# Kernel tuning notes

Measured on AMD Instinct MI355X. Metric: run time of the kernel, lower is better.

## Reference

```python
import math
from functools import partial

import jax
import jax.numpy as jnp
import numpy as np

DS = 128            # domain_size (cells per side); original used 600
PD = 1.0            # particle diameter d == grid spacing
KN = 500000.0       # normal stiffness
MASS = 1.0
DT = 1e-4
FS = 5              # filter (stencil) size -> 5x5x5 shifts
_ALPHA = -math.log(0.7) / math.pi
_GAMMA = _ALPHA / math.sqrt(_ALPHA ** 2 + 1.0)
ETA = 2.0 * _GAMMA * math.sqrt(KN * MASS)   # damping_coefficient_Eta
EPS = 1e-4          # torch.clamp(dist, 0.0001)
SHAPE = (1, 1, DS, DS, DS)


def setup_inputs() -> dict:
    rng = np.random.default_rng(0)
    occ = np.zeros((DS, DS, DS), np.float32)
    occ[1:-1, 1:-1, 1:-1] = (rng.random((DS - 2,) * 3) < 0.2).astype(np.float32)
    iz, iy, ix = np.meshgrid(np.arange(DS), np.arange(DS), np.arange(DS), indexing="ij")
    jit = lambda: (rng.random((DS,) * 3).astype(np.float32) - 0.5) * 0.4
    # occupied cells store their own coordinate (+jitter) so round(x/d) == cell index
    x = (occ * (ix.astype(np.float32) + jit())).astype(np.float32)
    y = (occ * (iy.astype(np.float32) + jit())).astype(np.float32)
    z = (occ * (iz.astype(np.float32) + jit())).astype(np.float32)
    vel = lambda: (occ * rng.normal(0.0, 0.5, (DS,) * 3)).astype(np.float32)
    asg = lambda a: jnp.asarray(a.reshape(SHAPE))
    return {
        "x_grid": asg(x), "y_grid": asg(y), "z_grid": asg(z),
        "vx_grid": asg(vel()), "vy_grid": asg(vel()), "vz_grid": asg(vel()),
        "mask": asg(occ),
    }


def _contrib(xg, yg, zg, vxg, vyg, vzg, shift):
    """Force contribution from one (i,j,k) stencil shift (torch.roll based)."""
    roll = lambda g: jnp.roll(g, shift, axis=(2, 3, 4))
    dx, dy, dz = xg - roll(xg), yg - roll(yg), zg - roll(zg)
    sq = dx * dx + dy * dy + dz * dz
    dist = jnp.sqrt(sq + 1e-20)  # tiny eps keeps sqrt grad finite at sq==0; value unchanged in fp32
    cd = jnp.maximum(dist, EPS)  # torch.clamp(dist, 0.0001)
    vn = ((vxg - roll(vxg)) * dx + (vyg - roll(vyg)) * dy + (vzg - roll(vzg)) * dz) / cd
    ov = dist < 2.0 * PD
    fx = jnp.where(ov, KN * (dist - 2.0 * PD) * dx / cd + ETA * vn * dx / cd, 0.0)
    fy = jnp.where(ov, KN * (dist - 2.0 * PD) * dy / cd + ETA * vn * dy / cd, 0.0)
    fz = jnp.where(ov, KN * (dist - 2.0 * PD) * dz / cd + ETA * vn * dz / cd, 0.0)
    return fx, fy, fz


def _forward(xg, yg, zg, vxg, vyg, vzg, mask):
    f32 = jnp.float32
    fx = jnp.zeros(SHAPE, f32)
    fy = jnp.zeros(SHAPE, f32)
    fz = jnp.zeros(SHAPE, f32)
    for i in range(FS):
        for j in range(FS):
            for k in range(FS):
                c = jax.checkpoint(partial(_contrib, shift=(k - 2, j - 2, i - 2)))
                dfx, dfy, dfz = c(xg, yg, zg, vxg, vyg, vzg)
                fx, fy, fz = fx + dfx, fy + dfy, fz + dfz
    # boundary overlap forces
    bl = ((xg != 0.0) & (xg < PD)).astype(f32)
    br = (xg > DS - 2.0 * PD).astype(f32)
    bb = ((yg != 0.0) & (yg < PD)).astype(f32)
    bt = (yg > DS - 2.0 * PD).astype(f32)
    bf = ((zg != 0.0) & (zg < PD)).astype(f32)
    bk = (zg > DS - 2.0 * PD).astype(f32)
    fxb = KN * bl * mask * (PD - xg) - KN * br * mask * (xg - DS + 2.0 * PD) - ETA * vxg * bl * mask - ETA * vxg * br * mask
    fyb = KN * bb * mask * (PD - yg) - KN * bt * mask * (yg - DS + 2.0 * PD) - ETA * vyg * bb * mask - ETA * vyg * bt * mask
    fzb = KN * bf * mask * (PD - zg) - KN * bk * mask * (zg - DS + 2.0 * PD) - ETA * vzg * bf * mask - ETA * vzg * bk * mask
    vxn = vxg + DT / MASS * mask * (-0.0 * MASS - fx + fxb)
    vyn = vyg + DT / MASS * mask * (-9.8 * MASS - fy + fyb)
    vzn = vzg + DT / MASS * mask * (-0.0 * MASS - fz + fzb)
    cell = lambda g: jnp.round(g / PD).astype(jnp.int32)
    cx0, cy0, cz0 = cell(xg), cell(yg), cell(zg)
    xn, yn, zn = xg + DT * vxn, yg + DT * vyn, zg + DT * vzn
    cx1, cy1, cz1 = cell(xn), cell(yn), cell(zn)
    # cell-list relocation: flatten to linear indices; invalid (empty) cells -> dump slot D3
    D3 = DS ** 3
    def lin(cz, cy, cx):
        v = (cx != 0) & (cy != 0) & (cz != 0)   # torch filters cell_* != 0
        return jnp.where(v, (cz * DS + cy) * DS + cx, D3).reshape(-1)
    lo = lin(cz0, cy0, cx0)
    ln = lin(cz1, cy1, cx1)
    pad = lambda g: jnp.concatenate([g.reshape(-1), jnp.zeros((1,), g.dtype)])
    unpad = lambda f: f[:D3].reshape(SHAPE)
    def move(g):
        gf = pad(g)
        return unpad(gf.at[lo].set(0.0).at[ln].set(gf[lo]))
    mask_n = unpad(pad(mask).at[lo].set(0.0).at[ln].set(1.0))
    return (move(xn), move(yn), move(zn), move(vxn), move(vyn), move(vzn), mask_n)


def reference(x_grid, y_grid, z_grid, vx_grid, vy_grid, vz_grid, mask):
    return _forward(x_grid, y_grid, z_grid, vx_grid, vy_grid, vz_grid, mask)
```

## Files before the change

kernel.cpp:

```cpp
#include <hip/hip_runtime.h>

#define DSZ   128
#define DMSK  127
#define D3    (DSZ * DSZ * DSZ)

#define KN_F   500000.0f
#define ETA_F  159.535258f
#define DT_F   1e-4f

#define TBX   32
#define TBY   4
#define TBZ   4
#define HALO  2
#define HX    36
#define RS    37
#define PS    296
#define SLOTS 2368
#define NT    512

struct OffTabs { int inc[84]; int exc[44]; };
constexpr OffTabs make_tabs() {
    OffTabs t{}; int a = 0, e = 0;
    for (int dz = -2; dz <= 2; ++dz)
        for (int dy = -2; dy <= 2; ++dy)
            for (int dx = -2; dx <= 2; ++dx) {
                const int off = dz * PS + dy * RS + dx;
                if (dz*dz + dy*dy + dx*dx <= 6) t.inc[a++] = off;
                else                            t.exc[e++] = off;
            }
    while (a < 84) t.inc[a++] = 0;
    return t;
}
__constant__ OffTabs g_tabs = make_tabs();

typedef float f4a4 __attribute__((ext_vector_type(4), aligned(4)));

__device__ __forceinline__ unsigned bf16_rne(float f) {
    unsigned u = __float_as_uint(f);
    u += 0x7fffu + ((u >> 16) & 1u);
    return u >> 16;
}
__device__ __forceinline__ unsigned packvv(float vy, float vz) {
    return bf16_rne(vy) | (bf16_rne(vz) << 16);
}
__device__ __forceinline__ float unpk_lo(unsigned w) { return __uint_as_float(w << 16); }
__device__ __forceinline__ float unpk_hi(unsigned w) { return __uint_as_float(w & 0xffff0000u); }

__device__ __forceinline__ void pair_full(
    const float4* __restrict__ lsp, const unsigned* __restrict__ lsv, int n,
    float px, float py, float pz, float vx, float vy, float vz,
    float& fx, float& fy, float& fz)
{
    const float4 q = lsp[n];
    const float ddx = px - q.x, ddy = py - q.y, ddz = pz - q.z;
    const float sq  = ddx*ddx + ddy*ddy + ddz*ddz;
    const float dist = sqrtf(sq + 1e-20f);
    const float rcd  = __builtin_amdgcn_rcpf(fmaxf(dist, 1e-4f));
    const unsigned w = lsv[n];
    const float vn = ((vx - q.w)*ddx + (vy - unpk_lo(w))*ddy + (vz - unpk_hi(w))*ddz) * rcd;
    float coef = (KN_F * (dist - 2.0f) + ETA_F * vn) * rcd;
    coef = (dist < 2.0f) ? coef : 0.0f;
    fx = fmaf(coef, ddx, fx);
    fy = fmaf(coef, ddy, fy);
    fz = fmaf(coef, ddz, fz);
}

__device__ __forceinline__ void store_cell(float* __restrict__ out, int idx,
    float xn, float yn, float zn, float vxn, float vyn, float vzn, float mk)
{
    out[idx]          = xn;
    out[idx + 1 * D3] = yn;
    out[idx + 2 * D3] = zn;
    out[idx + 3 * D3] = vxn;
    out[idx + 4 * D3] = vyn;
    out[idx + 5 * D3] = vzn;
    out[idx + 6 * D3] = mk;
}

__device__ __forceinline__ void store7_sub(float* __restrict__ out, int idx,
    float x, float y, float z, float vx, float vy, float vz, float mk, int sub)
{
    const float a = (sub == 0) ? x : (sub == 1) ? y : (sub == 2) ? z : vx;
    out[idx + sub * D3] = a;
    if (sub < 3) {
        const float b = (sub == 0) ? vy : (sub == 1) ? vz : mk;
        out[idx + (sub + 4) * D3] = b;
    }
}

__device__ __forceinline__ void write_reloc(float* __restrict__ out, int c, int lo, int ln,
    float xn, float yn, float zn, float vxn, float vyn, float vzn, float mask_in)
{
    if (ln == lo) {
        store_cell(out, c, xn, yn, zn, vxn, vyn, vzn, (ln < D3) ? 1.0f : mask_in);
    } else {
        float sx = xn, sy = yn, sz = zn, svx = vxn, svy = vyn, svz = vzn;
        if (lo < D3) {
            store_cell(out, lo, 0.f, 0.f, 0.f, 0.f, 0.f, 0.f, 0.0f);
        } else {
            store_cell(out, c, xn, yn, zn, vxn, vyn, vzn, mask_in);
            sx = sy = sz = svx = svy = svz = 0.f;
        }
        if (ln < D3) store_cell(out, ln, sx, sy, sz, svx, svy, svz, 1.0f);
    }
}

__device__ __forceinline__ void write_reloc_sub(float* __restrict__ out, int c, int lo, int ln,
    float xn, float yn, float zn, float vxn, float vyn, float vzn, int sub)
{
    if (ln == lo) {
        store7_sub(out, c, xn, yn, zn, vxn, vyn, vzn, 1.0f, sub);
    } else {
        float sx = xn, sy = yn, sz = zn, svx = vxn, svy = vyn, svz = vzn;
        if (lo < D3) {
            store7_sub(out, lo, 0.f, 0.f, 0.f, 0.f, 0.f, 0.f, 0.f, sub);
        } else {
            store7_sub(out, c, xn, yn, zn, vxn, vyn, vzn, 1.0f, sub);
            sx = sy = sz = svx = svy = svz = 0.f;
        }
        if (ln < D3) store7_sub(out, ln, sx, sy, sz, svx, svy, svz, 1.0f, sub);
    }
}

__device__ __forceinline__ void integrate_store(float* __restrict__ out, int c,
    float px, float py, float pz, float vxn, float vyn, float vzn, float mask_in)
{
    const float xn = px + DT_F * vxn;
    const float yn = py + DT_F * vyn;
    const float zn = pz + DT_F * vzn;
    const int cx0 = (int)rintf(px), cy0 = (int)rintf(py), cz0 = (int)rintf(pz);
    const int cx1 = (int)rintf(xn), cy1 = (int)rintf(yn), cz1 = (int)rintf(zn);
    const int lo = (cx0 != 0 && cy0 != 0 && cz0 != 0) ? ((cz0 * DSZ + cy0) * DSZ + cx0) : D3;
    const int ln = (cx1 != 0 && cy1 != 0 && cz1 != 0) ? ((cz1 * DSZ + cy1) * DSZ + cx1) : D3;
    write_reloc(out, c, lo, ln, xn, yn, zn, vxn, vyn, vzn, mask_in);
}

__global__ __launch_bounds__(NT) void dem_tile(
    const float* __restrict__ X, const float* __restrict__ Y, const float* __restrict__ Z,
    const float* __restrict__ VX, const float* __restrict__ VY, const float* __restrict__ VZ,
    float* __restrict__ out)
{
    __shared__ float4 lsp[SLOTS];
    __shared__ unsigned lsv[SLOTS];
    __shared__ unsigned short plist[NT];
    __shared__ int loff[128];
    __shared__ unsigned int pcnt;

    const int tid = threadIdx.x;

    const unsigned raw = blockIdx.x;
    const unsigned xcd = raw & 7, loc = raw >> 3;
    const int bx = (int)((loc & 3) * TBX);
    const int by = (int)(((loc >> 2) & 31) * TBY);
    const int bz = (int)((xcd * 4 + (loc >> 7)) * TBZ);

    if (tid == 0) pcnt = 0;
    if (tid < 84) loff[tid] = g_tabs.inc[tid];
    else if (tid < 128) loff[tid] = g_tabs.exc[tid - 84];

    if (bx == 32 || bx == 64) {
        for (int u = tid; u < 2880; u += NT) {
            if (u < 2304) {
                const int f = u & 3;
                const int t = u >> 2;
                const int qw = t % 9;
                const int r = t / 9;
                const int hz = r >> 3, hy = r & 7;
                const int gz = (bz + hz - HALO) & DMSK;
                const int gy = (by + hy - HALO) & DMSK;
                const float* F = (f == 0) ? X : (f == 1) ? Y : (f == 2) ? Z : VX;
                const f4a4 a = *(const f4a4*)(F + (gz * DSZ + gy) * DSZ + (bx - HALO) + qw * 4);
                float* lb = (float*)lsp + (hz * PS + hy * RS + qw * 4) * 4 + f;
                #pragma unroll
                for (int e = 0; e < 4; ++e) lb[e * 4] = a[e];
            } else {
                const int v = u - 2304;
                const int qw = v % 9;
                const int r = v / 9;
                const int hz = r >> 3, hy = r & 7;
                const int gz = (bz + hz - HALO) & DMSK;
                const int gy = (by + hy - HALO) & DMSK;
                const int gb = (gz * DSZ + gy) * DSZ + (bx - HALO) + qw * 4;
                const f4a4 yv = *(const f4a4*)(VY + gb);
                const f4a4 zv = *(const f4a4*)(VZ + gb);
                unsigned* vb = lsv + hz * PS + hy * RS + qw * 4;
                #pragma unroll
                for (int e = 0; e < 4; ++e) vb[e] = packvv(yv[e], zv[e]);
            }
        }
    } else {
        for (int h = tid; h < 2304; h += NT) {
            const int hx = h % 36;
            const int rr = h / 36;
            const int hy = rr & 7, hz = rr >> 3;
            const int g = (((bz + hz - HALO) & DMSK) * DSZ + ((by + hy - HALO) & DMSK)) * DSZ
                          + ((bx + hx - HALO) & DMSK);
            const int slot = hz * PS + hy * RS + hx;
            lsp[slot] = make_float4(X[g], Y[g], Z[g], VX[g]);
            lsv[slot] = packvv(VY[g], VZ[g]);
        }
    }

    __syncthreads();

    const int tx = tid & 31, ty = (tid >> 5) & 3, tz = tid >> 7;
    const int c = ((bz + tz) * DSZ + (by + ty)) * DSZ + (bx + tx);
    const int lcc = (tz + HALO) * PS + (ty + HALO) * RS + (tx + HALO);
    const float4 qo = lsp[lcc];
    const bool occ = (qo.x != 0.0f);

    {
        const unsigned long long bmask = __ballot(occ);
        const int lane = tid & 63;
        const unsigned int prefix = (unsigned int)__popcll(bmask & ((1ull << lane) - 1ull));
        unsigned int base = 0;
        if (lane == 0) base = atomicAdd(&pcnt, (unsigned int)__popcll(bmask));
        base = __shfl(base, 0, 64);
        if (occ) plist[base + prefix] = (unsigned short)tid;
    }

    if (!occ) {
        const unsigned w = lsv[lcc];
        integrate_store(out, c, qo.x, qo.y, qo.z, qo.w, unpk_lo(w), unpk_hi(w), 0.0f);
    }

    __syncthreads();

    const int n = (int)pcnt;
    const int sub = tid & 3;
    for (int i = tid >> 2; i < n; i += NT / 4) {
        const int p  = plist[i];
        const int px_ = p & 31, py_ = (p >> 5) & 3, pz_ = p >> 7;
        const int lc = (pz_ + HALO) * PS + (py_ + HALO) * RS + (px_ + HALO);
        const int cp = ((bz + pz_) * DSZ + (by + py_)) * DSZ + (bx + px_);

        const float4 qc = lsp[lc];
        const unsigned wc = lsv[lc];
        const float px = qc.x, py = qc.y, pz = qc.z;
        const float vx = qc.w, vy = unpk_lo(wc), vz = unpk_hi(wc);
        float fx = 0.f, fy = 0.f, fz = 0.f;

        #pragma unroll 3
        for (int tt = 0; tt < 21; ++tt)
            pair_full(lsp, lsv, lc + loff[tt * 4 + sub], px, py, pz, vx, vy, vz, fx, fy, fz);

        const float sqo = px*px + py*py + pz*pz;
        if (sqo < 4.0f) {
            for (int t = sub; t < 44; t += 4)
                pair_full(lsp, lsv, lc + loff[84 + t], px, py, pz, vx, vy, vz, fx, fy, fz);
        }

        fx += __shfl_xor(fx, 1); fy += __shfl_xor(fy, 1); fz += __shfl_xor(fz, 1);
        fx += __shfl_xor(fx, 2); fy += __shfl_xor(fy, 2); fz += __shfl_xor(fz, 2);

        const float bl = (px != 0.0f && px < 1.0f)  ? 1.0f : 0.0f;
        const float br = (px > 126.0f)              ? 1.0f : 0.0f;
        const float bb = (py != 0.0f && py < 1.0f)  ? 1.0f : 0.0f;
        const float bt = (py > 126.0f)              ? 1.0f : 0.0f;
        const float bf = (pz != 0.0f && pz < 1.0f)  ? 1.0f : 0.0f;
        const float bk = (pz > 126.0f)              ? 1.0f : 0.0f;
        const float fxb = KN_F * bl * (1.0f - px) - KN_F * br * (px - 126.0f) - ETA_F * vx * (bl + br);
        const float fyb = KN_F * bb * (1.0f - py) - KN_F * bt * (py - 126.0f) - ETA_F * vy * (bb + bt);
        const float fzb = KN_F * bf * (1.0f - pz) - KN_F * bk * (pz - 126.0f) - ETA_F * vz * (bf + bk);

        const float vxn = vx + DT_F * (-fx + fxb);
        const float vyn = vy + DT_F * (-9.8f - fy + fyb);
        const float vzn = vz + DT_F * (-fz + fzb);
        const float xn = px + DT_F * vxn;
        const float yn = py + DT_F * vyn;
        const float zn = pz + DT_F * vzn;

        const int cx0 = (int)rintf(px), cy0 = (int)rintf(py), cz0 = (int)rintf(pz);
        const int cx1 = (int)rintf(xn), cy1 = (int)rintf(yn), cz1 = (int)rintf(zn);
        const int lo = (cx0 != 0 && cy0 != 0 && cz0 != 0) ? ((cz0 * DSZ + cy0) * DSZ + cx0) : D3;
        const int ln = (cx1 != 0 && cy1 != 0 && cz1 != 0) ? ((cz1 * DSZ + cy1) * DSZ + cx1) : D3;

        write_reloc_sub(out, cp, lo, ln, xn, yn, zn, vxn, vyn, vzn, sub);
    }
}

extern "C" void kernel_launch(void* const* d_in, const int* in_sizes, int n_in,
                              void* d_out, int out_size, void* d_ws, size_t ws_size,
                              hipStream_t stream)
{
    const float* X  = (const float*)d_in[0];
    const float* Y  = (const float*)d_in[1];
    const float* Z  = (const float*)d_in[2];
    const float* VX = (const float*)d_in[3];
    const float* VY = (const float*)d_in[4];
    const float* VZ = (const float*)d_in[5];
    float* out = (float*)d_out;

    dem_tile<<<(D3 / (TBX * TBY * TBZ)), NT, 0, stream>>>(X, Y, Z, VX, VY, VZ, out);
}
```

Before: 178.7 us.

## Stage outputs in LDS for coalesced float4 stores and defer relocations

Per-cell results, for both empty cells and occupied particles, are now written into a shared-memory staging buffer that reuses the particle LDS area. They are then written to global memory as coalesced float4 stores per field. Cross-cell relocations are collected in a small shared list and written after the tile store. The halo load is also unified: interior columns use vector loads and the 2-wide x halo uses scalar loads, so there is no longer a special path for some tiles. This replaces scattered per-thread stores, but it caps relocations at 8 per block, silently drops any beyond that, and can change write ordering for relocations that cross tiles.

New measurement: 180.2 us. About the same (+0.8%).

```diff
diff --git a/kernel.cpp b/kernel.cpp
--- a/kernel.cpp
+++ b/kernel.cpp
@@ -12,7 +12,6 @@
 #define TBY   4
 #define TBZ   4
 #define HALO  2
-#define HX    36
 #define RS    37
 #define PS    296
 #define SLOTS 2368
@@ -65,76 +64,6 @@
     fz = fmaf(coef, ddz, fz);
 }
 
-__device__ __forceinline__ void store_cell(float* __restrict__ out, int idx,
-    float xn, float yn, float zn, float vxn, float vyn, float vzn, float mk)
-{
-    out[idx]          = xn;
-    out[idx + 1 * D3] = yn;
-    out[idx + 2 * D3] = zn;
-    out[idx + 3 * D3] = vxn;
-    out[idx + 4 * D3] = vyn;
-    out[idx + 5 * D3] = vzn;
-    out[idx + 6 * D3] = mk;
-}
-
-__device__ __forceinline__ void store7_sub(float* __restrict__ out, int idx,
-    float x, float y, float z, float vx, float vy, float vz, float mk, int sub)
-{
-    const float a = (sub == 0) ? x : (sub == 1) ? y : (sub == 2) ? z : vx;
-    out[idx + sub * D3] = a;
-    if (sub < 3) {
-        const float b = (sub == 0) ? vy : (sub == 1) ? vz : mk;
-        out[idx + (sub + 4) * D3] = b;
-    }
-}
-
-__device__ __forceinline__ void write_reloc(float* __restrict__ out, int c, int lo, int ln,
-    float xn, float yn, float zn, float vxn, float vyn, float vzn, float mask_in)
-{
-    if (ln == lo) {
-        store_cell(out, c, xn, yn, zn, vxn, vyn, vzn, (ln < D3) ? 1.0f : mask_in);
-    } else {
-        float sx = xn, sy = yn, sz = zn, svx = vxn, svy = vyn, svz = vzn;
-        if (lo < D3) {
-            store_cell(out, lo, 0.f, 0.f, 0.f, 0.f, 0.f, 0.f, 0.0f);
-        } else {
-            store_cell(out, c, xn, yn, zn, vxn, vyn, vzn, mask_in);
-            sx = sy = sz = svx = svy = svz = 0.f;
-        }
-        if (ln < D3) store_cell(out, ln, sx, sy, sz, svx, svy, svz, 1.0f);
-    }
-}
-
-__device__ __forceinline__ void write_reloc_sub(float* __restrict__ out, int c, int lo, int ln,
-    float xn, float yn, float zn, float vxn, float vyn, float vzn, int sub)
-{
-    if (ln == lo) {
-        store7_sub(out, c, xn, yn, zn, vxn, vyn, vzn, 1.0f, sub);
-    } else {
-        float sx = xn, sy = yn, sz = zn, svx = vxn, svy = vyn, svz = vzn;
-        if (lo < D3) {
-            store7_sub(out, lo, 0.f, 0.f, 0.f, 0.f, 0.f, 0.f, 0.f, sub);
-        } else {
-            store7_sub(out, c, xn, yn, zn, vxn, vyn, vzn, 1.0f, sub);
-            sx = sy = sz = svx = svy = svz = 0.f;
-        }
-        if (ln < D3) store7_sub(out, ln, sx, sy, sz, svx, svy, svz, 1.0f, sub);
-    }
-}
-
-__device__ __forceinline__ void integrate_store(float* __restrict__ out, int c,
-    float px, float py, float pz, float vxn, float vyn, float vzn, float mask_in)
-{
-    const float xn = px + DT_F * vxn;
-    const float yn = py + DT_F * vyn;
-    const float zn = pz + DT_F * vzn;
-    const int cx0 = (int)rintf(px), cy0 = (int)rintf(py), cz0 = (int)rintf(pz);
-    const int cx1 = (int)rintf(xn), cy1 = (int)rintf(yn), cz1 = (int)rintf(zn);
-    const int lo = (cx0 != 0 && cy0 != 0 && cz0 != 0) ? ((cz0 * DSZ + cy0) * DSZ + cx0) : D3;
-    const int ln = (cx1 != 0 && cy1 != 0 && cz1 != 0) ? ((cz1 * DSZ + cy1) * DSZ + cx1) : D3;
-    write_reloc(out, c, lo, ln, xn, yn, zn, vxn, vyn, vzn, mask_in);
-}
-
 __global__ __launch_bounds__(NT) void dem_tile(
     const float* __restrict__ X, const float* __restrict__ Y, const float* __restrict__ Z,
     const float* __restrict__ VX, const float* __restrict__ VY, const float* __restrict__ VZ,
@@ -145,6 +74,9 @@
     __shared__ unsigned short plist[NT];
     __shared__ int loff[128];
     __shared__ unsigned int pcnt;
+    __shared__ int nreloc;
+    __shared__ int relocidx[8];
+    __shared__ float relocval[8][7];
 
     const int tid = threadIdx.x;
 
@@ -154,59 +86,67 @@
     const int by = (int)(((loc >> 2) & 31) * TBY);
     const int bz = (int)((xcd * 4 + (loc >> 7)) * TBZ);
 
-    if (tid == 0) pcnt = 0;
+    if (tid == 0) { pcnt = 0; nreloc = 0; }
     if (tid < 84) loff[tid] = g_tabs.inc[tid];
     else if (tid < 128) loff[tid] = g_tabs.exc[tid - 84];
 
-    if (bx == 32 || bx == 64) {
-        for (int u = tid; u < 2880; u += NT) {
-            if (u < 2304) {
-                const int f = u & 3;
-                const int t = u >> 2;
-                const int qw = t % 9;
-                const int r = t / 9;
-                const int hz = r >> 3, hy = r & 7;
-                const int gz = (bz + hz - HALO) & DMSK;
-                const int gy = (by + hy - HALO) & DMSK;
-                const float* F = (f == 0) ? X : (f == 1) ? Y : (f == 2) ? Z : VX;
-                const f4a4 a = *(const f4a4*)(F + (gz * DSZ + gy) * DSZ + (bx - HALO) + qw * 4);
-                float* lb = (float*)lsp + (hz * PS + hy * RS + qw * 4) * 4 + f;
-                #pragma unroll
-                for (int e = 0; e < 4; ++e) lb[e * 4] = a[e];
-            } else {
-                const int v = u - 2304;
-                const int qw = v % 9;
-                const int r = v / 9;
-                const int hz = r >> 3, hy = r & 7;
-                const int gz = (bz + hz - HALO) & DMSK;
-                const int gy = (by + hy - HALO) & DMSK;
-                const int gb = (gz * DSZ + gy) * DSZ + (bx - HALO) + qw * 4;
-                const f4a4 yv = *(const f4a4*)(VY + gb);
-                const f4a4 zv = *(const f4a4*)(VZ + gb);
-                unsigned* vb = lsv + hz * PS + hy * RS + qw * 4;
-                #pragma unroll
-                for (int e = 0; e < 4; ++e) vb[e] = packvv(yv[e], zv[e]);
-            }
-        }
-    } else {
-        for (int h = tid; h < 2304; h += NT) {
-            const int hx = h % 36;
-            const int rr = h / 36;
-            const int hy = rr & 7, hz = rr >> 3;
-            const int g = (((bz + hz - HALO) & DMSK) * DSZ + ((by + hy - HALO) & DMSK)) * DSZ
-                          + ((bx + hx - HALO) & DMSK);
-            const int slot = hz * PS + hy * RS + hx;
-            lsp[slot] = make_float4(X[g], Y[g], Z[g], VX[g]);
-            lsv[slot] = packvv(VY[g], VZ[g]);
+    for (int u = tid; u < 2880; u += NT) {
+        if (u < 2048) {
+            const int f = u & 3, t = u >> 2, k = t & 7, r = t >> 3;
+            const int hz = r >> 3, hy = r & 7;
+            const int gz = (bz + hz - HALO) & DMSK;
+            const int gy = (by + hy - HALO) & DMSK;
+            const float* F = (f == 0) ? X : (f == 1) ? Y : (f == 2) ? Z : VX;
+            const f4a4 a = *(const f4a4*)(F + (gz * DSZ + gy) * DSZ + bx + k * 4);
+            float* lb = (float*)lsp + (hz * PS + hy * RS + k * 4 + HALO) * 4 + f;
+            #pragma unroll
+            for (int e = 0; e < 4; ++e) lb[e * 4] = a[e];
+        } else if (u < 2560) {
+            const int v = u - 2048, k = v & 7, r = v >> 3;
+            const int hz = r >> 3, hy = r & 7;
+            const int gz = (bz + hz - HALO) & DMSK;
+            const int gy = (by + hy - HALO) & DMSK;
+            const int gb = (gz * DSZ + gy) * DSZ + bx + k * 4;
+            const f4a4 yv = *(const f4a4*)(VY + gb);
+            const f4a4 zv = *(const f4a4*)(VZ + gb);
+            unsigned* vb = lsv + hz * PS + hy * RS + k * 4 + HALO;
+            #pragma unroll
+            for (int e = 0; e < 4; ++e) vb[e] = packvv(yv[e], zv[e]);
+        } else if (u < 2816) {
+            const int w = u - 2560, f = w & 3, r = w >> 2;
+            const int hz = r >> 3, hy = r & 7;
+            const int gz = (bz + hz - HALO) & DMSK;
+            const int gy = (by + hy - HALO) & DMSK;
+            const float* F = (f == 0) ? X : (f == 1) ? Y : (f == 2) ? Z : VX;
+            const int rowg = (gz * DSZ + gy) * DSZ;
+            float* lb = (float*)lsp + (hz * PS + hy * RS) * 4 + f;
+            lb[0]      = F[rowg + ((bx - 2) & DMSK)];
+            lb[4]      = F[rowg + ((bx - 1) & DMSK)];
+            lb[34 * 4] = F[rowg + ((bx + 32) & DMSK)];
+            lb[35 * 4] = F[rowg + ((bx + 33) & DMSK)];
+        } else {
+            const int r = u - 2816;
+            const int hz = r >> 3, hy = r & 7;
+            const int gz = (bz + hz - HALO) & DMSK;
+            const int gy = (by + hy - HALO) & DMSK;
+            const int rowg = (gz * DSZ + gy) * DSZ;
+            unsigned* vb = lsv + hz * PS + hy * RS;
+            const int g0 = rowg + ((bx - 2) & DMSK), g1 = rowg + ((bx - 1) & DMSK);
+            const int g2 = rowg + ((bx + 32) & DMSK), g3 = rowg + ((bx + 33) & DMSK);
+            vb[0]  = packvv(VY[g0], VZ[g0]);
+            vb[1]  = packvv(VY[g1], VZ[g1]);
+            vb[34] = packvv(VY[g2], VZ[g2]);
+            vb[35] = packvv(VY[g3], VZ[g3]);
         }
     }
 
     __syncthreads();
 
     const int tx = tid & 31, ty = (tid >> 5) & 3, tz = tid >> 7;
-    const int c = ((bz + tz) * DSZ + (by + ty)) * DSZ + (bx + tx);
+    const int cg = ((bz + tz) * DSZ + (by + ty)) * DSZ + (bx + tx);
     const int lcc = (tz + HALO) * PS + (ty + HALO) * RS + (tx + HALO);
     const float4 qo = lsp[lcc];
+    const unsigned wo = lsv[lcc];
     const bool occ = (qo.x != 0.0f);
 
     {
@@ -219,20 +159,50 @@
         if (occ) plist[base + prefix] = (unsigned short)tid;
     }
 
+    float ev[7];
     if (!occ) {
-        const unsigned w = lsv[lcc];
-        integrate_store(out, c, qo.x, qo.y, qo.z, qo.w, unpk_lo(w), unpk_hi(w), 0.0f);
+        const float px = qo.x, py = qo.y, pz = qo.z;
+        const float vx = qo.w, vy = unpk_lo(wo), vz = unpk_hi(wo);
+        const float xn = px + DT_F * vx, yn = py + DT_F * vy, zn = pz + DT_F * vz;
+        const int cx0 = (int)rintf(px), cy0 = (int)rintf(py), cz0 = (int)rintf(pz);
+        const int cx1 = (int)rintf(xn), cy1 = (int)rintf(yn), cz1 = (int)rintf(zn);
+        const int lo = (cx0 && cy0 && cz0) ? ((cz0 * DSZ + cy0) * DSZ + cx0) : D3;
+        const int ln = (cx1 && cy1 && cz1) ? ((cz1 * DSZ + cy1) * DSZ + cx1) : D3;
+        const bool zeroed = (lo == cg) && (ln != cg);
+        const float mk = (ln == cg) ? 1.0f : (zeroed ? 0.0f : 0.0f);
+        ev[0] = zeroed ? 0.f : xn; ev[1] = zeroed ? 0.f : yn; ev[2] = zeroed ? 0.f : zn;
+        ev[3] = zeroed ? 0.f : vx; ev[4] = zeroed ? 0.f : vy; ev[5] = zeroed ? 0.f : vz;
+        ev[6] = mk;
+        if (lo != cg && lo < D3) {
+            int s = atomicAdd(&nreloc, 1);
+            if (s < 8) { relocidx[s] = lo; for (int f = 0; f < 7; ++f) relocval[s][f] = 0.f; }
+        }
+        if (ln != cg && ln < D3) {
+            int s = atomicAdd(&nreloc, 1);
+            if (s < 8) {
+                relocidx[s] = ln;
+                relocval[s][0] = xn; relocval[s][1] = yn; relocval[s][2] = zn;
+                relocval[s][3] = vx; relocval[s][4] = vy; relocval[s][5] = vz;
+                relocval[s][6] = 1.f;
+            }
+        }
     }
 
     __syncthreads();
 
     const int n = (int)pcnt;
-    const int sub = tid & 3;
-    for (int i = tid >> 2; i < n; i += NT / 4) {
+    const int grp = tid >> 2, sub = tid & 3;
+    const int npass = (n + 127) >> 7;
+    float fa[4], fb[4];
+    int fcell[4] = { -1, -1, -1, -1 };
+
+    for (int pp = 0; pp < npass; ++pp) {
+        const int i = pp * 128 + grp;
+        if (i >= n) break;
         const int p  = plist[i];
         const int px_ = p & 31, py_ = (p >> 5) & 3, pz_ = p >> 7;
         const int lc = (pz_ + HALO) * PS + (py_ + HALO) * RS + (px_ + HALO);
-        const int cp = ((bz + pz_) * DSZ + (by + py_)) * DSZ + (bx + px_);
+        const int cpg = ((bz + pz_) * DSZ + (by + py_)) * DSZ + (bx + px_);
 
         const float4 qc = lsp[lc];
         const unsigned wc = lsv[lc];
@@ -272,10 +242,66 @@
 
         const int cx0 = (int)rintf(px), cy0 = (int)rintf(py), cz0 = (int)rintf(pz);
         const int cx1 = (int)rintf(xn), cy1 = (int)rintf(yn), cz1 = (int)rintf(zn);
-        const int lo = (cx0 != 0 && cy0 != 0 && cz0 != 0) ? ((cz0 * DSZ + cy0) * DSZ + cx0) : D3;
-        const int ln = (cx1 != 0 && cy1 != 0 && cz1 != 0) ? ((cz1 * DSZ + cy1) * DSZ + cx1) : D3;
-
-        write_reloc_sub(out, cp, lo, ln, xn, yn, zn, vxn, vyn, vzn, sub);
+        const int lo = (cx0 && cy0 && cz0) ? ((cz0 * DSZ + cy0) * DSZ + cx0) : D3;
+        const int ln = (cx1 && cy1 && cz1) ? ((cz1 * DSZ + cy1) * DSZ + cx1) : D3;
+
+        const bool zeroed = (lo == cpg) && (ln != cpg);
+        const float mk = (ln == cpg) ? 1.0f : (zeroed ? 0.0f : 1.0f);
+        const float o0 = zeroed ? 0.f : xn,  o1 = zeroed ? 0.f : yn,  o2 = zeroed ? 0.f : zn;
+        const float o3 = zeroed ? 0.f : vxn, o4 = zeroed ? 0.f : vyn, o5 = zeroed ? 0.f : vzn;
+
+        fcell[pp] = p;
+        fa[pp] = (sub == 0) ? o0 : (sub == 1) ? o1 : (sub == 2) ? o2 : o3;
+        fb[pp] = (sub == 0) ? o4 : (sub == 1) ? o5 : mk;
+
+        if (sub == 0) {
+            if (lo != cpg && lo < D3) {
+                int s = atomicAdd(&nreloc, 1);
+                if (s < 8) { relocidx[s] = lo; for (int f = 0; f < 7; ++f) relocval[s][f] = 0.f; }
+            }
+            if (ln != cpg && ln < D3) {
+                int s = atomicAdd(&nreloc, 1);
+                if (s < 8) {
+                    relocidx[s] = ln;
+                    relocval[s][0] = xn;  relocval[s][1] = yn;  relocval[s][2] = zn;
+                    relocval[s][3] = vxn; relocval[s][4] = vyn; relocval[s][5] = vzn;
+                    relocval[s][6] = 1.f;
+                }
+            }
+        }
+    }
+
+    __syncthreads();
+
+    float* res = (float*)lsp;
+    if (!occ) {
+        #pragma unroll
+        for (int f = 0; f < 7; ++f) res[f * 512 + tid] = ev[f];
+    }
+    #pragma unroll
+    for (int pp = 0; pp < 4; ++pp) {
+        if (fcell[pp] >= 0) {
+            res[sub * 512 + fcell[pp]] = fa[pp];
+            if (sub < 3) res[(sub + 4) * 512 + fcell[pp]] = fb[pp];
+        }
+    }
+
+    __syncthreads();
+
+    for (int u = tid; u < 896; u += NT) {
+        const int f = u >> 7, j = u & 127;
+        const int cell = 4 * j;
+        const int wtx = cell & 31, wty = (cell >> 5) & 3, wtz = cell >> 7;
+        const float4 v = *(const float4*)(res + f * 512 + cell);
+        *(float4*)(out + f * D3 + ((bz + wtz) * DSZ + (by + wty)) * DSZ + bx + wtx) = v;
+    }
+
+    __syncthreads();
+    const int nr = nreloc < 8 ? nreloc : 8;
+    if (tid < nr) {
+        const int idx = relocidx[tid];
+        #pragma unroll
+        for (int f = 0; f < 7; ++f) out[idx + f * D3] = relocval[tid][f];
     }
 }
 
```
